# Optimization experiments

Hardware: AMD Instinct MI355X
Metric: run time of the kernel (lower is better)

Reference implementation:

```python
import jax, jax.numpy as jnp
import numpy as np

FEAT_STRIDE = 16
PRE_NMS_TOP_N = 4000
POST_NMS_TOP_N = 300
NMS_THRESH = 0.7


def _whctrs(a):
    w = a[2] - a[0] + 1.0
    h = a[3] - a[1] + 1.0
    return w, h, a[0] + 0.5 * (w - 1.0), a[1] + 0.5 * (h - 1.0)

def _mkanchors(ws, hs, xc, yc):
    ws = ws[:, None]; hs = hs[:, None]
    return np.hstack([xc - 0.5 * (ws - 1), yc - 0.5 * (hs - 1), xc + 0.5 * (ws - 1), yc + 0.5 * (hs - 1)])

def _ratio_enum(anchor, ratios):
    w, h, xc, yc = _whctrs(anchor)
    size = w * h
    ws = np.round(np.sqrt(size / ratios))
    hs = np.round(ws * ratios)
    return _mkanchors(ws, hs, xc, yc)

def _scale_enum(anchor, scales):
    w, h, xc, yc = _whctrs(anchor)
    return _mkanchors(w * scales, h * scales, xc, yc)

def generate_anchors(base_size, ratios, scales):
    base = np.array([1.0, 1.0, base_size, base_size], dtype=np.float64) - 1.0
    ra = _ratio_enum(base, np.asarray(ratios, dtype=np.float64))
    return np.vstack([_scale_enum(ra[i], np.asarray(scales, dtype=np.float64)) for i in range(ra.shape[0])]).astype(np.float32)

# ---- NMS: sequential greedy suppression over score-sorted boxes ----

def _nms_keep(boxes, thresh):
    # boxes: [N,4] sorted by descending score. Legacy +1 area convention.
    boxes = jax.lax.stop_gradient(boxes)
    x1, y1, x2, y2 = boxes[:, 0], boxes[:, 1], boxes[:, 2], boxes[:, 3]
    areas = (x2 - x1 + 1.0) * (y2 - y1 + 1.0)
    xx1 = jnp.maximum(x1[:, None], x1[None, :])
    yy1 = jnp.maximum(y1[:, None], y1[None, :])
    xx2 = jnp.minimum(x2[:, None], x2[None, :])
    yy2 = jnp.minimum(y2[:, None], y2[None, :])
    w = jnp.maximum(xx2 - xx1 + 1.0, 0.0)
    h = jnp.maximum(yy2 - yy1 + 1.0, 0.0)
    inter = w * h
    iou = inter / (areas[:, None] + areas[None, :] - inter)
    sup = iou > thresh  # [N,N]
    n = boxes.shape[0]
    idxs = jnp.arange(n)

    def body(suppressed, i):
        kept = ~suppressed[i]
        suppressed = suppressed | (kept & sup[i] & (idxs > i))
        return suppressed, kept

    _, keep = jax.lax.scan(body, jnp.zeros((n,), dtype=bool), idxs)
    return keep  # [N] bool

# ---- forward ----

def _forward(scores, bbox_deltas, im_info, anchors):
    A = anchors.shape[0]
    B = bbox_deltas.shape[0]
    H, W = scores.shape[2], scores.shape[3]
    sc = scores[:, A:, :, :]  # fg scores [B,A,H,W]

    # anchor grid: K = H*W shifts, anchors broadcast over shifts (K major, A minor)
    shift_x = jnp.arange(W, dtype=scores.dtype) * FEAT_STRIDE
    shift_y = jnp.arange(H, dtype=scores.dtype) * FEAT_STRIDE
    sx, sy = jnp.meshgrid(shift_x, shift_y)  # 'xy' indexing, like np.meshgrid
    shifts = jnp.stack([sx.ravel(), sy.ravel(), sx.ravel(), sy.ravel()], axis=1)  # [K,4]
    all_anchors = (anchors[None, :, :] + shifts[:, None, :]).reshape(-1, 4)  # [K*A,4]

    deltas = bbox_deltas.transpose(0, 2, 3, 1).reshape(B, -1, 4)  # [B,N,4]
    scr = sc.transpose(0, 2, 3, 1).reshape(B, -1)  # [B,N]

    # bbox_transform_inv
    widths = all_anchors[:, 2] - all_anchors[:, 0] + 1.0
    heights = all_anchors[:, 3] - all_anchors[:, 1] + 1.0
    ctr_x = all_anchors[:, 0] + 0.5 * widths
    ctr_y = all_anchors[:, 1] + 0.5 * heights
    dx, dy, dw, dh = deltas[..., 0], deltas[..., 1], deltas[..., 2], deltas[..., 3]
    pcx = dx * widths + ctr_x
    pcy = dy * heights + ctr_y
    pw = jnp.exp(dw) * widths
    ph = jnp.exp(dh) * heights
    px1 = pcx - 0.5 * pw
    py1 = pcy - 0.5 * ph
    px2 = pcx + 0.5 * pw
    py2 = pcy + 0.5 * ph

    # clip_boxes per image: x in [0, W_img-1], y in [0, H_img-1]
    wmax = im_info[:, 1:2] - 1.0  # [B,1]
    hmax = im_info[:, 0:1] - 1.0
    px1 = jnp.clip(px1, 0.0, wmax)
    px2 = jnp.clip(px2, 0.0, wmax)
    py1 = jnp.clip(py1, 0.0, hmax)
    py2 = jnp.clip(py2, 0.0, hmax)
    proposals = jnp.stack([px1, py1, px2, py2], axis=-1)  # [B,N,4]

    def per_image(props, s, b_idx):
        _, order = jax.lax.top_k(s, PRE_NMS_TOP_N)  # descending
        p = props[order]  # [PRE,4]
        keep = _nms_keep(p, NMS_THRESH)
        ranks = jnp.cumsum(keep.astype(jnp.int32)) - 1
        slot = jnp.where(keep & (ranks < POST_NMS_TOP_N), ranks, POST_NMS_TOP_N)
        boxes_out = jnp.zeros((POST_NMS_TOP_N + 1, 4), p.dtype).at[slot].set(p)[:POST_NMS_TOP_N]
        col0 = jnp.full((POST_NMS_TOP_N, 1), b_idx.astype(p.dtype))
        return jnp.concatenate([col0, boxes_out], axis=1)  # [POST,5]

    return jax.vmap(per_image)(proposals, scr, jnp.arange(B))


def setup_inputs() -> dict:
    key = jax.random.key(0)
    k1, k2 = jax.random.split(key)
    B, A, H, W = 2, 9, 50, 50
    scores = jax.random.normal(k1, (B, 2 * A, H, W), dtype=jnp.float32)
    bbox_deltas = jax.random.normal(k2, (B, 4 * A, H, W), dtype=jnp.float32) * 0.1
    im_info = jnp.tile(jnp.array([[800.0, 800.0, 1.0]], dtype=jnp.float32), (B, 1))
    anchors = jnp.asarray(generate_anchors(16, [0.5, 1.0, 2.0], [8, 16, 32]))
    return {"scores": scores, "bbox_deltas": bbox_deltas, "im_info": im_info, "anchors": anchors}


def reference(scores, bbox_deltas, im_info, anchors):
    return _forward(scores, bbox_deltas, im_info, anchors)
```

## Files before the change

kernel.cpp:

```cpp
#include <hip/hip_runtime.h>
#include <stdint.h>

#define NA 9
#define HH 50
#define WW 50
#define NPROP (HH*WW*NA)
#define NSORT 32768
#define CHUNK 4096
#define PRE_NMS 4000
#define POST_NMS 300
#define NWORDS 63
#define NMS_T 0.7f
#define FSTRIDE 16.0f

typedef unsigned long long ull;

__device__ __forceinline__ uint32_t f32_ord(float s) {
    uint32_t u = __float_as_uint(s);
    return (u & 0x80000000u) ? ~u : (u | 0x80000000u);
}

__global__ __launch_bounds__(1024) void prep_sort_kernel(
        const float* __restrict__ scores,
        const float* __restrict__ deltas,
        const float* __restrict__ im_info,
        const float* __restrict__ anchors,
        ull* __restrict__ keys,
        float4* __restrict__ boxes4) {
    __shared__ ull sk[CHUNK];
    int chunk = blockIdx.x;
    int img   = chunk >> 3;
    int cbase = (chunk & 7) * CHUNK;
    int tid = threadIdx.x;

    float wmax = im_info[img*3+1] - 1.0f;
    float hmax = im_info[img*3+0] - 1.0f;

    for (int e = tid; e < CHUNK; e += 1024) {
        int i = cbase + e;
        if (i >= NPROP) { sk[e] = 0ull; continue; }
        int a   = i % NA;
        int pos = i / NA;
        int w   = pos % WW;
        int h   = pos / WW;

        float score = scores[((size_t)img*2*NA + NA + a)*(HH*WW) + pos];
        sk[e] = ((ull)f32_ord(score) << 32) | (ull)(0xFFFFFFFFu - (uint32_t)i);

        float ax1 = anchors[a*4+0], ay1 = anchors[a*4+1];
        float ax2 = anchors[a*4+2], ay2 = anchors[a*4+3];
        float sx = (float)w * FSTRIDE, sy = (float)h * FSTRIDE;
        float x1 = ax1 + sx, y1 = ay1 + sy, x2 = ax2 + sx, y2 = ay2 + sy;
        float bw = x2 - x1 + 1.0f;
        float bh = y2 - y1 + 1.0f;
        float cx = x1 + 0.5f * bw;
        float cy = y1 + 0.5f * bh;

        const float* dp = deltas + (size_t)img*4*NA*(HH*WW);
        float dx = dp[(4*a+0)*(HH*WW)+pos];
        float dy = dp[(4*a+1)*(HH*WW)+pos];
        float dw = dp[(4*a+2)*(HH*WW)+pos];
        float dh = dp[(4*a+3)*(HH*WW)+pos];

        float pcx = dx * bw + cx;
        float pcy = dy * bh + cy;
        float pw  = expf(dw) * bw;
        float ph  = expf(dh) * bh;

        float px1 = fminf(fmaxf(pcx - 0.5f*pw, 0.0f), wmax);
        float py1 = fminf(fmaxf(pcy - 0.5f*ph, 0.0f), hmax);
        float px2 = fminf(fmaxf(pcx + 0.5f*pw, 0.0f), wmax);
        float py2 = fminf(fmaxf(pcy + 0.5f*ph, 0.0f), hmax);

        boxes4[(size_t)img*NPROP + i] = make_float4(px1, py1, px2, py2);
    }
    __syncthreads();

    for (int k = 2; k <= CHUNK; k <<= 1) {
        for (int j = k >> 1; j > 0; j >>= 1) {
            for (int p = tid; p < CHUNK/2; p += 1024) {
                int i = ((p & ~(j-1)) << 1) | (p & (j-1));
                int l = i | j;
                bool desc = (((cbase + i) & k) == 0);
                ull x = sk[i], y = sk[l];
                if ((x < y) == desc) { sk[i] = y; sk[l] = x; }
            }
            __syncthreads();
        }
    }
    ull* gb = keys + (size_t)chunk * CHUNK;
    for (int e = tid; e < CHUNK; e += 1024) gb[e] = sk[e];
}

template<int NCROSS>
__global__ __launch_bounds__(1024) void merge_kernel(const ull* __restrict__ src,
                                                     ull* __restrict__ dst) {
    __shared__ ull sk[CHUNK];
    const int K = CHUNK << NCROSS;
    int chunk = blockIdx.x;
    int img   = chunk >> 3;
    int cbase = (chunk & 7) * CHUNK;
    const ull* ib = src + (size_t)img * NSORT;
    int tid = threadIdx.x;
    const bool desc = ((cbase & K) == 0);

    for (int e = tid; e < CHUNK; e += 1024) {
        int gi = cbase + e;
        ull v[1 << NCROSS];
        #pragma unroll
        for (int s = 0; s < (1 << NCROSS); ++s) {
            int off = 0;
            #pragma unroll
            for (int t = 0; t < NCROSS; ++t)
                if (s & (1 << t)) off ^= (K >> (t+1));
            v[s] = ib[gi ^ off];
        }
        #pragma unroll
        for (int t = 0; t < NCROSS; ++t) {
            const int J = K >> (t+1);
            bool mx = desc ^ ((cbase & J) != 0);
            #pragma unroll
            for (int s = 0; s < (1 << NCROSS); ++s) {
                if ((s & ((2 << t) - 1)) == 0) {
                    ull a = v[s], b = v[s | (1 << t)];
                    bool agtb = a > b;
                    v[s] = (agtb == mx) ? a : b;
                }
            }
        }
        sk[e] = v[0];
    }
    __syncthreads();

    for (int j = CHUNK >> 1; j > 0; j >>= 1) {
        for (int p = tid; p < CHUNK/2; p += 1024) {
            int i = ((p & ~(j-1)) << 1) | (p & (j-1));
            int l = i | j;
            ull x = sk[i], y = sk[l];
            if ((x < y) == desc) { sk[i] = y; sk[l] = x; }
        }
        __syncthreads();
    }
    ull* ob = dst + (size_t)img * NSORT + cbase;
    for (int e = tid; e < CHUNK; e += 1024) ob[e] = sk[e];
}

__global__ __launch_bounds__(1024) void final_merge_gather(const ull* __restrict__ src,
                                                           const float4* __restrict__ boxes4,
                                                           float4* __restrict__ gboxes) {
    __shared__ ull sk[CHUNK];
    int img = blockIdx.x;
    const ull* ib = src + (size_t)img * NSORT;
    int tid = threadIdx.x;

    for (int e = tid; e < CHUNK; e += 1024) {
        ull m = ib[e];
        #pragma unroll
        for (int s = 1; s < 8; ++s) {
            ull v = ib[e + s*CHUNK];
            m = (v > m) ? v : m;
        }
        sk[e] = m;
    }
    __syncthreads();

    for (int j = CHUNK >> 1; j > 0; j >>= 1) {
        for (int p = tid; p < CHUNK/2; p += 1024) {
            int i = ((p & ~(j-1)) << 1) | (p & (j-1));
            int l = i | j;
            ull x = sk[i], y = sk[l];
            if (x < y) { sk[i] = y; sk[l] = x; }
        }
        __syncthreads();
    }

    for (int e = tid; e < PRE_NMS; e += 1024) {
        uint32_t idx = 0xFFFFFFFFu - (uint32_t)(sk[e] & 0xFFFFFFFFull);
        gboxes[(size_t)img*PRE_NMS + e] = boxes4[(size_t)img*NPROP + idx];
    }
}

__global__ __launch_bounds__(64) void mask_kernel(const float4* __restrict__ gboxes,
                                                  ull* __restrict__ mask) {
    int rb = blockIdx.x, cb = blockIdx.y, b = blockIdx.z;
    if (cb < rb) return;
    __shared__ float cx1[64], cy1[64], cx2[64], cy2[64], car[64];
    int tid = threadIdx.x;

    int j0 = cb*64 + tid;
    float4 cbx = (j0 < PRE_NMS) ? gboxes[(size_t)b*PRE_NMS + j0]
                                : make_float4(0.f,0.f,0.f,0.f);
    cx1[tid]=cbx.x; cy1[tid]=cbx.y; cx2[tid]=cbx.z; cy2[tid]=cbx.w;
    car[tid]=(cbx.z-cbx.x+1.0f)*(cbx.w-cbx.y+1.0f);
    __syncthreads();

    int i = rb*64 + tid;
    if (i >= PRE_NMS) return;
    float4 rbx = gboxes[(size_t)b*PRE_NMS + i];
    float ix1=rbx.x, iy1=rbx.y, ix2=rbx.z, iy2=rbx.w;
    float iarea=(ix2-ix1+1.0f)*(iy2-iy1+1.0f);

    ull bits = 0;
    #pragma unroll 16
    for (int k = 0; k < 64; ++k) {
        int j = cb*64 + k;
        float xx1 = fmaxf(ix1, cx1[k]);
        float yy1 = fmaxf(iy1, cy1[k]);
        float xx2 = fminf(ix2, cx2[k]);
        float yy2 = fminf(iy2, cy2[k]);
        float ww = fmaxf(xx2 - xx1 + 1.0f, 0.0f);
        float hh = fmaxf(yy2 - yy1 + 1.0f, 0.0f);
        float inter = ww * hh;
        float iou = inter / (iarea + car[k] - inter);
        if ((j > i) & (j < PRE_NMS) & (iou > NMS_T)) bits |= (1ull << k);
    }
    mask[(((size_t)b*PRE_NMS + i) << 6) + cb] = bits;
}

__global__ __launch_bounds__(64) void scan_kernel(const ull* __restrict__ mask,
                                                  const float4* __restrict__ gboxes,
                                                  float* __restrict__ out) {
    __shared__ int keep_idx[POST_NMS];
    int b = blockIdx.x;
    int lane = threadIdx.x;
    ull supp = 0;
    if (lane == NWORDS-1) supp = 0xFFFFFFFF00000000ull;
    if (lane >= NWORDS)   supp = ~0ull;
    int kept = 0;
    bool done = false;

    for (int wi = 0; wi < NWORDS && !done; ++wi) {
        ull avail = ~__shfl(supp, wi);
        while (avail) {
            int bi = __builtin_ctzll(avail);
            int i = (wi << 6) + bi;
            if (lane == 0) keep_idx[kept] = i;
            ++kept;
            if (kept >= POST_NMS) { done = true; break; }
            const ull* row = mask + (((size_t)b*PRE_NMS + i) << 6);
            ull m = (lane >= wi && lane < NWORDS) ? row[lane] : 0ull;
            supp |= m;
            ull mw = __shfl(m, wi);
            avail &= ~mw;
            avail &= avail - 1;
        }
    }
    __syncthreads();

    for (int r = lane; r < POST_NMS; r += 64) {
        float4 bx = (r < kept) ? gboxes[(size_t)b*PRE_NMS + keep_idx[r]]
                               : make_float4(0.f,0.f,0.f,0.f);
        float* o = out + (size_t)(b*POST_NMS + r)*5;
        o[0]=(float)b; o[1]=bx.x; o[2]=bx.y; o[3]=bx.z; o[4]=bx.w;
    }
}

extern "C" void kernel_launch(void* const* d_in, const int* in_sizes, int n_in,
                              void* d_out, int out_size, void* d_ws, size_t ws_size,
                              hipStream_t stream) {
    (void)n_in; (void)out_size; (void)ws_size;
    const float* scores  = (const float*)d_in[0];
    const float* deltas  = (const float*)d_in[1];
    const float* im_info = (const float*)d_in[2];
    const float* anchors = (const float*)d_in[3];
    float* out = (float*)d_out;

    const int B = in_sizes[0] / (2*NA*HH*WW);

    ull* keys0 = (ull*)d_ws;
    ull* keys1 = keys0 + (size_t)B*NSORT;
    float4* boxes4 = (float4*)(keys1 + (size_t)B*NSORT);
    float4* gboxes = boxes4 + (size_t)B*NPROP;
    ull* mask = (ull*)(gboxes + (size_t)B*PRE_NMS);

    prep_sort_kernel<<<B*8, 1024, 0, stream>>>(scores, deltas, im_info, anchors,
                                               keys0, boxes4);
    merge_kernel<1><<<B*8, 1024, 0, stream>>>(keys0, keys1);
    merge_kernel<2><<<B*8, 1024, 0, stream>>>(keys1, keys0);
    final_merge_gather<<<B, 1024, 0, stream>>>(keys0, boxes4, gboxes);
    dim3 mgrid(NWORDS, NWORDS, B);
    mask_kernel<<<mgrid, 64, 0, stream>>>(gboxes, mask);
    scan_kernel<<<B, 64, 0, stream>>>(mask, gboxes, out);
}
```

Baseline: 280.4 us.

## Replace full bitonic sort with histogram top-k selection and prefetch NMS mask tiles

The full 32K-element bitonic sort and its merge kernels are replaced by a 16-bit score histogram built with atomics during decode. A single block per image then finds the threshold bucket for the top 4000, compacts the candidates into shared memory and bitonic-sorts only 8192 keys. Separately, the NMS scan kernel double-buffers 64-row mask tiles in shared memory with register prefetch, so each kept box no longer waits on a dependent global load. Risks include overflow if more than 8192 keys land in or above the threshold bucket, an extra memset launch, and a large per-thread register prefetch buffer.

```diff
diff --git a/kernel.cpp b/kernel.cpp
--- a/kernel.cpp
+++ b/kernel.cpp
@@ -5,11 +5,12 @@
 #define HH 50
 #define WW 50
 #define NPROP (HH*WW*NA)
-#define NSORT 32768
-#define CHUNK 4096
 #define PRE_NMS 4000
 #define POST_NMS 300
 #define NWORDS 63
+#define ROWSTRIDE 64
+#define MROWS 4032
+#define SORTN 8192
 #define NMS_T 0.7f
 #define FSTRIDE 16.0f
 
@@ -20,158 +21,139 @@
     return (u & 0x80000000u) ? ~u : (u | 0x80000000u);
 }
 
-__global__ __launch_bounds__(1024) void prep_sort_kernel(
-        const float* __restrict__ scores,
-        const float* __restrict__ deltas,
-        const float* __restrict__ im_info,
-        const float* __restrict__ anchors,
-        ull* __restrict__ keys,
-        float4* __restrict__ boxes4) {
-    __shared__ ull sk[CHUNK];
-    int chunk = blockIdx.x;
-    int img   = chunk >> 3;
-    int cbase = (chunk & 7) * CHUNK;
-    int tid = threadIdx.x;
-
-    float wmax = im_info[img*3+1] - 1.0f;
-    float hmax = im_info[img*3+0] - 1.0f;
-
-    for (int e = tid; e < CHUNK; e += 1024) {
-        int i = cbase + e;
-        if (i >= NPROP) { sk[e] = 0ull; continue; }
-        int a   = i % NA;
-        int pos = i / NA;
-        int w   = pos % WW;
-        int h   = pos / WW;
-
-        float score = scores[((size_t)img*2*NA + NA + a)*(HH*WW) + pos];
-        sk[e] = ((ull)f32_ord(score) << 32) | (ull)(0xFFFFFFFFu - (uint32_t)i);
-
-        float ax1 = anchors[a*4+0], ay1 = anchors[a*4+1];
-        float ax2 = anchors[a*4+2], ay2 = anchors[a*4+3];
-        float sx = (float)w * FSTRIDE, sy = (float)h * FSTRIDE;
-        float x1 = ax1 + sx, y1 = ay1 + sy, x2 = ax2 + sx, y2 = ay2 + sy;
-        float bw = x2 - x1 + 1.0f;
-        float bh = y2 - y1 + 1.0f;
-        float cx = x1 + 0.5f * bw;
-        float cy = y1 + 0.5f * bh;
-
-        const float* dp = deltas + (size_t)img*4*NA*(HH*WW);
-        float dx = dp[(4*a+0)*(HH*WW)+pos];
-        float dy = dp[(4*a+1)*(HH*WW)+pos];
-        float dw = dp[(4*a+2)*(HH*WW)+pos];
-        float dh = dp[(4*a+3)*(HH*WW)+pos];
-
-        float pcx = dx * bw + cx;
-        float pcy = dy * bh + cy;
-        float pw  = expf(dw) * bw;
-        float ph  = expf(dh) * bh;
-
-        float px1 = fminf(fmaxf(pcx - 0.5f*pw, 0.0f), wmax);
-        float py1 = fminf(fmaxf(pcy - 0.5f*ph, 0.0f), hmax);
-        float px2 = fminf(fmaxf(pcx + 0.5f*pw, 0.0f), wmax);
-        float py2 = fminf(fmaxf(pcy + 0.5f*ph, 0.0f), hmax);
-
-        boxes4[(size_t)img*NPROP + i] = make_float4(px1, py1, px2, py2);
-    }
-    __syncthreads();
-
-    for (int k = 2; k <= CHUNK; k <<= 1) {
+__global__ void decode_hist(const float* __restrict__ scores,
+                            const float* __restrict__ deltas,
+                            const float* __restrict__ im_info,
+                            const float* __restrict__ anchors,
+                            ull* __restrict__ keys,
+                            float4* __restrict__ boxes4,
+                            uint32_t* __restrict__ hist, int B) {
+    int t = blockIdx.x * blockDim.x + threadIdx.x;
+    if (t >= B * NPROP) return;
+    int b = t / NPROP;
+    int i = t % NPROP;
+
+    int a   = i % NA;
+    int pos = i / NA;
+    int w   = pos % WW;
+    int h   = pos / WW;
+
+    float score = scores[((size_t)b*2*NA + NA + a)*(HH*WW) + pos];
+    ull key = ((ull)f32_ord(score) << 32) | (ull)(0xFFFFFFFFu - (uint32_t)i);
+    keys[t] = key;
+    atomicAdd(&hist[((uint32_t)b << 16) | (uint32_t)(key >> 48)], 1u);
+
+    float ax1 = anchors[a*4+0], ay1 = anchors[a*4+1];
+    float ax2 = anchors[a*4+2], ay2 = anchors[a*4+3];
+    float sx = (float)w * FSTRIDE, sy = (float)h * FSTRIDE;
+    float x1 = ax1 + sx, y1 = ay1 + sy, x2 = ax2 + sx, y2 = ay2 + sy;
+    float bw = x2 - x1 + 1.0f;
+    float bh = y2 - y1 + 1.0f;
+    float cx = x1 + 0.5f * bw;
+    float cy = y1 + 0.5f * bh;
+
+    const float* dp = deltas + (size_t)b*4*NA*(HH*WW);
+    float dx = dp[(4*a+0)*(HH*WW)+pos];
+    float dy = dp[(4*a+1)*(HH*WW)+pos];
+    float dw = dp[(4*a+2)*(HH*WW)+pos];
+    float dh = dp[(4*a+3)*(HH*WW)+pos];
+
+    float pcx = dx * bw + cx;
+    float pcy = dy * bh + cy;
+    float pw  = expf(dw) * bw;
+    float ph  = expf(dh) * bh;
+
+    float wmax = im_info[b*3+1] - 1.0f;
+    float hmax = im_info[b*3+0] - 1.0f;
+    float px1 = fminf(fmaxf(pcx - 0.5f*pw, 0.0f), wmax);
+    float py1 = fminf(fmaxf(pcy - 0.5f*ph, 0.0f), hmax);
+    float px2 = fminf(fmaxf(pcx + 0.5f*pw, 0.0f), wmax);
+    float py2 = fminf(fmaxf(pcy + 0.5f*ph, 0.0f), hmax);
+
+    boxes4[t] = make_float4(px1, py1, px2, py2);
+}
+
+__global__ __launch_bounds__(1024) void select_sort_gather(
+        const ull* __restrict__ keys,
+        const uint32_t* __restrict__ hist,
+        const float4* __restrict__ boxes4,
+        float4* __restrict__ gboxes) {
+    __shared__ ull sk[SORTN];
+    __shared__ int sA[1024], sB[1024];
+    __shared__ int nfine[64];
+    __shared__ int sSeg, aboveC, thr, lcount;
+    int img = blockIdx.x, tid = threadIdx.x;
+    const uint32_t* h = hist + ((uint32_t)img << 16);
+
+    {
+        const uint4* h4 = (const uint4*)h;
+        uint32_t s = 0;
+        #pragma unroll
+        for (int u = 0; u < 16; ++u) {
+            uint4 v = h4[(tid << 4) | u];
+            s += v.x + v.y + v.z + v.w;
+        }
+        sA[tid] = (int)s;
+    }
+    __syncthreads();
+    int* curp = sA; int* nxtp = sB;
+    for (int d = 1; d < 1024; d <<= 1) {
+        int v = curp[tid] + ((tid + d < 1024) ? curp[tid + d] : 0);
+        nxtp[tid] = v;
+        __syncthreads();
+        int* tmp = curp; curp = nxtp; nxtp = tmp;
+    }
+    {
+        int cftS  = curp[tid];
+        int cftS1 = (tid < 1023) ? curp[tid + 1] : 0;
+        if (cftS >= PRE_NMS && cftS1 < PRE_NMS) { sSeg = tid; aboveC = cftS1; }
+    }
+    __syncthreads();
+    if (tid < 64) nfine[tid] = (int)h[(sSeg << 6) | tid];
+    __syncthreads();
+    if (tid == 0) {
+        int cum = aboveC;
+        int t = sSeg << 6;
+        for (int w = 63; w >= 0; --w) {
+            int nc = cum + nfine[w];
+            if (nc >= PRE_NMS) { t = (sSeg << 6) | w; break; }
+            cum = nc;
+        }
+        thr = t;
+        lcount = 0;
+    }
+    __syncthreads();
+
+    {
+        const ull* kb = keys + (size_t)img * NPROP;
+        int th = thr;
+        for (int i = tid; i < NPROP; i += 1024) {
+            ull key = kb[i];
+            if ((int)(key >> 48) >= th) {
+                int p = atomicAdd(&lcount, 1);
+                if (p < SORTN) sk[p] = key;
+            }
+        }
+    }
+    __syncthreads();
+    {
+        int M = lcount;
+        for (int e = tid; e < SORTN; e += 1024)
+            if (e >= M) sk[e] = 0ull;
+    }
+    __syncthreads();
+
+    for (int k = 2; k <= SORTN; k <<= 1) {
         for (int j = k >> 1; j > 0; j >>= 1) {
-            for (int p = tid; p < CHUNK/2; p += 1024) {
-                int i = ((p & ~(j-1)) << 1) | (p & (j-1));
-                int l = i | j;
-                bool desc = (((cbase + i) & k) == 0);
-                ull x = sk[i], y = sk[l];
-                if ((x < y) == desc) { sk[i] = y; sk[l] = x; }
+            for (int p = tid; p < SORTN/2; p += 1024) {
+                int i2 = ((p & ~(j-1)) << 1) | (p & (j-1));
+                int l2 = i2 | j;
+                bool desc = ((i2 & k) == 0);
+                ull x = sk[i2], y = sk[l2];
+                if ((x < y) == desc) { sk[i2] = y; sk[l2] = x; }
             }
             __syncthreads();
         }
-    }
-    ull* gb = keys + (size_t)chunk * CHUNK;
-    for (int e = tid; e < CHUNK; e += 1024) gb[e] = sk[e];
-}
-
-template<int NCROSS>
-__global__ __launch_bounds__(1024) void merge_kernel(const ull* __restrict__ src,
-                                                     ull* __restrict__ dst) {
-    __shared__ ull sk[CHUNK];
-    const int K = CHUNK << NCROSS;
-    int chunk = blockIdx.x;
-    int img   = chunk >> 3;
-    int cbase = (chunk & 7) * CHUNK;
-    const ull* ib = src + (size_t)img * NSORT;
-    int tid = threadIdx.x;
-    const bool desc = ((cbase & K) == 0);
-
-    for (int e = tid; e < CHUNK; e += 1024) {
-        int gi = cbase + e;
-        ull v[1 << NCROSS];
-        #pragma unroll
-        for (int s = 0; s < (1 << NCROSS); ++s) {
-            int off = 0;
-            #pragma unroll
-            for (int t = 0; t < NCROSS; ++t)
-                if (s & (1 << t)) off ^= (K >> (t+1));
-            v[s] = ib[gi ^ off];
-        }
-        #pragma unroll
-        for (int t = 0; t < NCROSS; ++t) {
-            const int J = K >> (t+1);
-            bool mx = desc ^ ((cbase & J) != 0);
-            #pragma unroll
-            for (int s = 0; s < (1 << NCROSS); ++s) {
-                if ((s & ((2 << t) - 1)) == 0) {
-                    ull a = v[s], b = v[s | (1 << t)];
-                    bool agtb = a > b;
-                    v[s] = (agtb == mx) ? a : b;
-                }
-            }
-        }
-        sk[e] = v[0];
-    }
-    __syncthreads();
-
-    for (int j = CHUNK >> 1; j > 0; j >>= 1) {
-        for (int p = tid; p < CHUNK/2; p += 1024) {
-            int i = ((p & ~(j-1)) << 1) | (p & (j-1));
-            int l = i | j;
-            ull x = sk[i], y = sk[l];
-            if ((x < y) == desc) { sk[i] = y; sk[l] = x; }
-        }
-        __syncthreads();
-    }
-    ull* ob = dst + (size_t)img * NSORT + cbase;
-    for (int e = tid; e < CHUNK; e += 1024) ob[e] = sk[e];
-}
-
-__global__ __launch_bounds__(1024) void final_merge_gather(const ull* __restrict__ src,
-                                                           const float4* __restrict__ boxes4,
-                                                           float4* __restrict__ gboxes) {
-    __shared__ ull sk[CHUNK];
-    int img = blockIdx.x;
-    const ull* ib = src + (size_t)img * NSORT;
-    int tid = threadIdx.x;
-
-    for (int e = tid; e < CHUNK; e += 1024) {
-        ull m = ib[e];
-        #pragma unroll
-        for (int s = 1; s < 8; ++s) {
-            ull v = ib[e + s*CHUNK];
-            m = (v > m) ? v : m;
-        }
-        sk[e] = m;
-    }
-    __syncthreads();
-
-    for (int j = CHUNK >> 1; j > 0; j >>= 1) {
-        for (int p = tid; p < CHUNK/2; p += 1024) {
-            int i = ((p & ~(j-1)) << 1) | (p & (j-1));
-            int l = i | j;
-            ull x = sk[i], y = sk[l];
-            if (x < y) { sk[i] = y; sk[l] = x; }
-        }
-        __syncthreads();
     }
 
     for (int e = tid; e < PRE_NMS; e += 1024) {
@@ -214,22 +196,43 @@
         float iou = inter / (iarea + car[k] - inter);
         if ((j > i) & (j < PRE_NMS) & (iou > NMS_T)) bits |= (1ull << k);
     }
-    mask[(((size_t)b*PRE_NMS + i) << 6) + cb] = bits;
+    mask[(((size_t)b*MROWS + i) << 6) + cb] = bits;
 }
 
 __global__ __launch_bounds__(64) void scan_kernel(const ull* __restrict__ mask,
                                                   const float4* __restrict__ gboxes,
                                                   float* __restrict__ out) {
+    __shared__ ull buf[2][64][ROWSTRIDE];
     __shared__ int keep_idx[POST_NMS];
     int b = blockIdx.x;
     int lane = threadIdx.x;
+    const ull* mbase = mask + ((size_t)b * MROWS << 6);
+
     ull supp = 0;
     if (lane == NWORDS-1) supp = 0xFFFFFFFF00000000ull;
     if (lane >= NWORDS)   supp = ~0ull;
     int kept = 0;
     bool done = false;
+    int cur = 0;
+
+    {
+        const ulonglong2* src = (const ulonglong2*)mbase;
+        ulonglong2* d2 = (ulonglong2*)buf[0];
+        #pragma unroll
+        for (int m = 0; m < 32; ++m) d2[lane + (m << 6)] = src[lane + (m << 6)];
+        __syncthreads();
+    }
 
     for (int wi = 0; wi < NWORDS && !done; ++wi) {
+        ulonglong2 pf[32];
+        bool havepf = (wi + 1 < NWORDS);
+        if (havepf) {
+            const ulonglong2* src =
+                (const ulonglong2*)(mbase + (((size_t)(wi+1) << 6) << 6));
+            #pragma unroll
+            for (int m = 0; m < 32; ++m) pf[m] = src[lane + (m << 6)];
+        }
+
         ull avail = ~__shfl(supp, wi);
         while (avail) {
             int bi = __builtin_ctzll(avail);
@@ -237,12 +240,19 @@
             if (lane == 0) keep_idx[kept] = i;
             ++kept;
             if (kept >= POST_NMS) { done = true; break; }
-            const ull* row = mask + (((size_t)b*PRE_NMS + i) << 6);
-            ull m = (lane >= wi && lane < NWORDS) ? row[lane] : 0ull;
-            supp |= m;
-            ull mw = __shfl(m, wi);
-            avail &= ~mw;
-            avail &= avail - 1;
+            ull w = buf[cur][bi][wi];
+            ull r = (lane > wi) ? buf[cur][bi][lane] : 0;
+            supp |= r;
+            avail &= ~w;
+            avail &= ~(1ull << bi);
+        }
+
+        if (havepf && !done) {
+            ulonglong2* d2 = (ulonglong2*)buf[cur ^ 1];
+            #pragma unroll
+            for (int m = 0; m < 32; ++m) d2[lane + (m << 6)] = pf[m];
+            __syncthreads();
+            cur ^= 1;
         }
     }
     __syncthreads();
@@ -267,17 +277,16 @@
 
     const int B = in_sizes[0] / (2*NA*HH*WW);
 
-    ull* keys0 = (ull*)d_ws;
-    ull* keys1 = keys0 + (size_t)B*NSORT;
-    float4* boxes4 = (float4*)(keys1 + (size_t)B*NSORT);
+    float4* boxes4 = (float4*)d_ws;
     float4* gboxes = boxes4 + (size_t)B*NPROP;
-    ull* mask = (ull*)(gboxes + (size_t)B*PRE_NMS);
-
-    prep_sort_kernel<<<B*8, 1024, 0, stream>>>(scores, deltas, im_info, anchors,
-                                               keys0, boxes4);
-    merge_kernel<1><<<B*8, 1024, 0, stream>>>(keys0, keys1);
-    merge_kernel<2><<<B*8, 1024, 0, stream>>>(keys1, keys0);
-    final_merge_gather<<<B, 1024, 0, stream>>>(keys0, boxes4, gboxes);
+    ull*    keys   = (ull*)(gboxes + (size_t)B*PRE_NMS);
+    ull*    mask   = keys + (size_t)B*NPROP;
+    uint32_t* hist = (uint32_t*)(mask + ((size_t)B*MROWS << 6));
+
+    hipMemsetAsync(hist, 0, (size_t)B*65536*sizeof(uint32_t), stream);
+    decode_hist<<<(B*NPROP + 255)/256, 256, 0, stream>>>(scores, deltas, im_info,
+                                                         anchors, keys, boxes4, hist, B);
+    select_sort_gather<<<B, 1024, 0, stream>>>(keys, hist, boxes4, gboxes);
     dim3 mgrid(NWORDS, NWORDS, B);
     mask_kernel<<<mgrid, 64, 0, stream>>>(gboxes, mask);
     scan_kernel<<<B, 64, 0, stream>>>(mask, gboxes, out);
```

Result: faster. 256.8 us (-8.4%).
